# Performance work log

Measured on AMD Instinct MI355X. Metric: run time of the kernel, lower is better.

## Reference

```python
import jax, jax.numpy as jnp
import numpy as np
import math

N_NODES = 50000
N_EDGES = 800000
IN_DIM = 128
OUT_DIM = 64
TIME_DIM = 128


def setup_inputs() -> dict:
    key = jax.random.key(0)
    ks = jax.random.split(key, 9)
    return {
        "node_feats": jax.random.normal(ks[0], (N_NODES, IN_DIM), dtype=jnp.float32),
        "time_diff": jax.random.uniform(ks[1], (N_EDGES,), dtype=jnp.float32),
        "src": jax.random.randint(ks[2], (N_EDGES,), 0, N_NODES, dtype=jnp.int32),
        "dst": jax.random.randint(ks[3], (N_EDGES,), 0, N_NODES, dtype=jnp.int32),
        "W": jax.random.normal(ks[4], (OUT_DIM, IN_DIM), dtype=jnp.float32) * 0.05,
        "Wv": jax.random.normal(ks[5], (OUT_DIM, IN_DIM), dtype=jnp.float32) * 0.05,
        "omega": jax.random.normal(ks[6], (TIME_DIM // 2,), dtype=jnp.float32),
        "Wt": jax.random.normal(ks[7], (OUT_DIM, TIME_DIM), dtype=jnp.float32) * 0.05,
        "a": jax.random.normal(ks[8], (3 * OUT_DIM,), dtype=jnp.float32) * 0.05,
    }


def reference(node_feats, time_diff, src, dst, W, Wv, omega, Wt, a):
    N = node_feats.shape[0]
    d = W.shape[0]  # out_dim
    time_dim = 2 * omega.shape[0]

    # gather + linear projections per edge
    h_src = node_feats[src] @ W.T          # [E, d]
    h_dst = node_feats[dst] @ W.T          # [E, d]
    v_src = node_feats[src] @ Wv.T         # [E, d]

    # temporal encoding: interleaved sin/cos of t * omega, scaled by sqrt(1/dim)
    ang = time_diff[:, None] * omega[None, :]                       # [E, dim/2]
    pe = jnp.stack([jnp.sin(ang), jnp.cos(ang)], axis=-1)
    pe = pe.reshape(ang.shape[0], time_dim) * jnp.float32(math.sqrt(1.0 / time_dim))
    t_emb = pe @ Wt.T                                               # [E, d]

    # attn_fc(concat([h_src, h_dst, t_emb])) == split dot products (same math, no big concat)
    e = h_src @ a[:d] + h_dst @ a[d:2 * d] + t_emb @ a[2 * d:]      # [E]
    e = jnp.where(e > 0, e, 0.2 * e)  # LeakyReLU(0.2)

    # edge_softmax: softmax over incoming edges of each destination node
    m = jax.ops.segment_max(e, dst, num_segments=N)
    ex = jnp.exp(e - m[dst])
    den = jax.ops.segment_sum(ex, dst, num_segments=N)
    alpha = ex / den[dst]  # dropout is identity in eval mode

    # weighted message scatter-sum aggregation
    msg = v_src * alpha[:, None]                                    # [E, d]
    return jax.ops.segment_sum(msg, dst, num_segments=N)            # [N, d]
```

## Files before the change

kernel.cpp:

```cpp
#include <hip/hip_runtime.h>
#include <hip/hip_bf16.h>
#include <hip/hip_fp16.h>
#include <math.h>

#define IN_DIM   128
#define OUT_DIM  64
#define THALF    64
#define PE_SCALE 0.08838834764831845f
#define TBL      2048

typedef __attribute__((ext_vector_type(8))) short  short8;
typedef __attribute__((ext_vector_type(4))) float  f32x4;

__device__ inline unsigned short bf16_rne(float x) {
    unsigned u = __float_as_uint(x);
    return (unsigned short)((u + 0x7FFFu + ((u >> 16) & 1u)) >> 16);
}

__global__ __launch_bounds__(256) void k_prep(
    const float* __restrict__ W, const float* __restrict__ Wt,
    const float* __restrict__ a, const float* __restrict__ Wv,
    const float* __restrict__ omega,
    float* __restrict__ gtab, unsigned short* __restrict__ Bp,
    int* __restrict__ cnt, int* __restrict__ pref, int N)
{
    __shared__ float satv[IN_DIM];
    __shared__ float saW1[IN_DIM], saW2[IN_DIM];
    int t = threadIdx.x;
    if (t < IN_DIM) {
        float x3 = 0.f;
        for (int j = 0; j < OUT_DIM; ++j)
            x3 += a[2 * OUT_DIM + j] * Wt[j * IN_DIM + t];
        satv[t] = x3;
        if (blockIdx.x == 0) {
            float x1 = 0.f, x2 = 0.f;
            for (int j = 0; j < OUT_DIM; ++j) {
                float wj = W[j * IN_DIM + t];
                x1 += a[j] * wj;
                x2 += a[OUT_DIM + j] * wj;
            }
            saW1[t] = x1; saW2[t] = x2;
        }
    }
    __syncthreads();

    int idx = blockIdx.x * 256 + t;
    if (idx <= TBL) {
        float tt = (float)idx * (1.0f / TBL);
        float acc = 0.f;
#pragma unroll
        for (int i = 0; i < THALF; ++i) {
            float sp, cp;
            __sincosf(tt * omega[i], &sp, &cp);
            acc += sp * satv[2 * i] + cp * satv[2 * i + 1];
        }
        gtab[idx] = acc;
    }
    if (idx < 64) pref[idx] = 0;
    for (int i = idx; i < N; i += gridDim.x * 256) cnt[i] = 0;

    if (blockIdx.x == 0) {
        for (int i = t; i < 5 * 4 * 64 * 8; i += 256) {
            int j    = i & 7;
            int lane = (i >> 3) & 63;
            int k0i  = (i >> 9) & 3;
            int tt   = i >> 11;
            int kk = k0i * 32 + (lane >> 4) * 8 + j;
            int n  = lane & 15;
            float val;
            if (tt < 4)     val = Wv[(tt * 16 + n) * IN_DIM + kk];
            else            val = (n == 0) ? saW1[kk] : (n == 1) ? saW2[kk] : 0.f;
            Bp[i] = bf16_rne(val);
        }
    }
}

__global__ __launch_bounds__(256) void k_node_mfma(
    const float* __restrict__ feats,
    const unsigned short* __restrict__ Bp,
    unsigned short* __restrict__ vb,
    float* __restrict__ s1,
    float* __restrict__ s2,
    int N)
{
    int gwave = (blockIdx.x * 256 + threadIdx.x) >> 6;
    int lane  = threadIdx.x & 63;
    int ntiles = (N + 15) >> 4;
    if (gwave >= ntiles) return;
    int row = lane & 15, quad = lane >> 4;
    int nodeA = gwave * 16 + row;
    int nodeL = nodeA < N ? nodeA : N - 1;

    const float* arow = feats + (size_t)nodeL * IN_DIM + quad * 8;
    short8 afrag[4];
#pragma unroll
    for (int k0i = 0; k0i < 4; ++k0i) {
        float4 fa = *(const float4*)(arow + k0i * 32);
        float4 fb = *(const float4*)(arow + k0i * 32 + 4);
        union { unsigned u[4]; short8 s; } cv;
        cv.u[0] = (__float_as_uint(fa.x) >> 16) | (__float_as_uint(fa.y) & 0xFFFF0000u);
        cv.u[1] = (__float_as_uint(fa.z) >> 16) | (__float_as_uint(fa.w) & 0xFFFF0000u);
        cv.u[2] = (__float_as_uint(fb.x) >> 16) | (__float_as_uint(fb.y) & 0xFFFF0000u);
        cv.u[3] = (__float_as_uint(fb.z) >> 16) | (__float_as_uint(fb.w) & 0xFFFF0000u);
        afrag[k0i] = cv.s;
    }

    const short8* B8 = (const short8*)Bp;
    f32x4 acc[5];
#pragma unroll
    for (int t = 0; t < 5; ++t) acc[t] = (f32x4){0.f, 0.f, 0.f, 0.f};
#pragma unroll
    for (int t = 0; t < 5; ++t) {
#pragma unroll
        for (int k0i = 0; k0i < 4; ++k0i)
            acc[t] = __builtin_amdgcn_mfma_f32_16x16x32_bf16(
                afrag[k0i], B8[(t * 4 + k0i) * 64 + lane], acc[t], 0, 0, 0);
    }

    int col = lane & 15;
    int baseNode = gwave * 16 + quad * 4;
#pragma unroll
    for (int r = 0; r < 4; ++r) {
        int nd = baseNode + r;
        if (nd < N) {
            unsigned short* vr = vb + (size_t)nd * OUT_DIM + col;
#pragma unroll
            for (int t = 0; t < 4; ++t) vr[t * 16] = bf16_rne(acc[t][r]);
            if (col == 0)      s1[nd] = acc[4][r];
            else if (col == 1) s2[nd] = acc[4][r];
        }
    }
}

__global__ __launch_bounds__(256) void k_logits_rank(
    const float* __restrict__ tdiff,
    const int* __restrict__ src,
    const int* __restrict__ dst,
    const float* __restrict__ gtab,
    const float* __restrict__ s1,
    const float* __restrict__ s2,
    int* __restrict__ cnt,
    int2* __restrict__ rp,
    int E)
{
    int base = (blockIdx.x * 256 + threadIdx.x) * 8;
    if (base >= E) return;
    if (base + 8 <= E) {
        int4   sa = *(const int4*)(src + base);
        int4   sb = *(const int4*)(src + base + 4);
        int4   da = *(const int4*)(dst + base);
        int4   db = *(const int4*)(dst + base + 4);
        float4 ta = *(const float4*)(tdiff + base);
        float4 tb = *(const float4*)(tdiff + base + 4);
        int s[8]   = {sa.x, sa.y, sa.z, sa.w, sb.x, sb.y, sb.z, sb.w};
        int d[8]   = {da.x, da.y, da.z, da.w, db.x, db.y, db.z, db.w};
        float tv[8] = {ta.x, ta.y, ta.z, ta.w, tb.x, tb.y, tb.z, tb.w};

        int rk[8];
#pragma unroll
        for (int i = 0; i < 8; ++i) rk[i] = atomicAdd(cnt + d[i], 1);

        unsigned pw[8];
#pragma unroll
        for (int i = 0; i < 8; ++i) {
            float a1 = s1[s[i]];
            float a2 = s2[d[i]];
            float x = tv[i] * (float)TBL;
            int i0 = (int)x;
            i0 = i0 < 0 ? 0 : (i0 > TBL - 1 ? TBL - 1 : i0);
            float fr = x - (float)i0;
            float ev = a1 + a2 + PE_SCALE * (gtab[i0] + fr * (gtab[i0 + 1] - gtab[i0]));
            ev = ev > 0.f ? ev : 0.2f * ev;
            pw[i] = ((unsigned)s[i] << 16) | (unsigned)__half_as_ushort(__float2half(ev));
        }
#pragma unroll
        for (int i = 0; i < 4; ++i)
            *(int4*)(rp + base + 2 * i) =
                make_int4(rk[2 * i], (int)pw[2 * i], rk[2 * i + 1], (int)pw[2 * i + 1]);
    } else {
        for (int e = base; e < E; ++e) {
            int s = src[e], d = dst[e];
            int rk = atomicAdd(cnt + d, 1);
            float a1 = s1[s], a2 = s2[d];
            float x = tdiff[e] * (float)TBL;
            int i0 = (int)x;
            i0 = i0 < 0 ? 0 : (i0 > TBL - 1 ? TBL - 1 : i0);
            float fr = x - (float)i0;
            float ev = a1 + a2 + PE_SCALE * (gtab[i0] + fr * (gtab[i0 + 1] - gtab[i0]));
            ev = ev > 0.f ? ev : 0.2f * ev;
            unsigned pw = ((unsigned)s << 16) | (unsigned)__half_as_ushort(__float2half(ev));
            rp[e] = make_int2(rk, (int)pw);
        }
    }
}

__global__ __launch_bounds__(256) void k_scan1(const int* __restrict__ cnt,
                                               int* __restrict__ offs,
                                               int* __restrict__ pref, int N)
{
    __shared__ int lds[256];
    int b = blockIdx.x, t = threadIdx.x;
    int base = b * 1024 + t * 4;
    int v0 = (base + 0 < N) ? cnt[base + 0] : 0;
    int v1 = (base + 1 < N) ? cnt[base + 1] : 0;
    int v2 = (base + 2 < N) ? cnt[base + 2] : 0;
    int v3 = (base + 3 < N) ? cnt[base + 3] : 0;
    int s = v0 + v1 + v2 + v3;
    lds[t] = s;
    __syncthreads();
    for (int off = 1; off < 256; off <<= 1) {
        int tmp = (t >= off) ? lds[t - off] : 0;
        __syncthreads();
        lds[t] += tmp;
        __syncthreads();
    }
    int ex = lds[t] - s;
    if (base + 0 < N) offs[base + 0] = ex;
    ex += v0;
    if (base + 1 < N) offs[base + 1] = ex;
    ex += v1;
    if (base + 2 < N) offs[base + 2] = ex;
    ex += v2;
    if (base + 3 < N) offs[base + 3] = ex;
    int total = lds[255];
    if (t > b && t < (int)gridDim.x) atomicAdd(pref + t, total);
}

__global__ __launch_bounds__(256) void k_scatter(
    const int* __restrict__ dst,
    const int2* __restrict__ rp,
    const int* __restrict__ offs,
    const int* __restrict__ pref,
    unsigned* __restrict__ payload,
    int E)
{
    int base = (blockIdx.x * 256 + threadIdx.x) * 8;
    if (base >= E) return;
    if (base + 8 <= E) {
        int4 da = *(const int4*)(dst + base);
        int4 db = *(const int4*)(dst + base + 4);
        int d[8] = {da.x, da.y, da.z, da.w, db.x, db.y, db.z, db.w};
        int4 v0 = *(const int4*)(rp + base);
        int4 v1 = *(const int4*)(rp + base + 2);
        int4 v2 = *(const int4*)(rp + base + 4);
        int4 v3 = *(const int4*)(rp + base + 6);
        int rk[8] = {v0.x, v0.z, v1.x, v1.z, v2.x, v2.z, v3.x, v3.z};
        int pw[8] = {v0.y, v0.w, v1.y, v1.w, v2.y, v2.w, v3.y, v3.w};
        int o[8];
#pragma unroll
        for (int i = 0; i < 8; ++i) o[i] = offs[d[i]] + pref[d[i] >> 10] + rk[i];
#pragma unroll
        for (int i = 0; i < 8; ++i) payload[o[i]] = (unsigned)pw[i];
    } else {
        for (int e = base; e < E; ++e) {
            int d = dst[e];
            int2 v = rp[e];
            payload[offs[d] + pref[d >> 10] + v.x] = (unsigned)v.y;
        }
    }
}

__global__ __launch_bounds__(256) void k_aggregate(
    const int* __restrict__ offs,
    const int* __restrict__ pref,
    const unsigned* __restrict__ payload,
    const unsigned short* __restrict__ vb,
    float* __restrict__ out,
    int N, int E)
{
    int wid  = (blockIdx.x * blockDim.x + threadIdx.x) >> 6;
    int lane = threadIdx.x & 63;
    if (wid >= N) return;
    int beg = offs[wid] + pref[wid >> 10];
    int end = (wid + 1 < N) ? (offs[wid + 1] + pref[(wid + 1) >> 10]) : E;
    int deg = end - beg;
    int g8 = lane >> 3, r = lane & 7;

    float acc[8];
#pragma unroll
    for (int i = 0; i < 8; ++i) acc[i] = 0.f;
    float den = 0.f;

    for (int base = 0; base < deg; base += 64) {
        int cl = deg - base; if (cl > 64) cl = 64;
        bool valid = lane < cl;
        unsigned pl = valid ? payload[beg + base + lane] : 0u;
        float ex = valid ? __expf(__half2float(__ushort_as_half((unsigned short)(pl & 0xFFFFu)))) : 0.f;
        int   sv = valid ? (int)(pl >> 16) : 0;

        float sum = ex;
#pragma unroll
        for (int off = 32; off; off >>= 1) sum += __shfl_xor(sum, off, 64);
        den += sum;

        int rounds = (cl + 15) >> 4;
        for (int j = 0; j < rounds; ++j) {
            int i0 = j * 16 + g8;
            int i1 = i0 + 8;
            float e0 = __shfl(ex, i0, 64);
            int   s0 = __shfl(sv, i0, 64);
            float e1 = __shfl(ex, i1, 64);
            int   s1v = __shfl(sv, i1, 64);
            uint4 w0 = *((const uint4*)(vb + (size_t)s0 * OUT_DIM) + r);
            uint4 w1 = *((const uint4*)(vb + (size_t)s1v * OUT_DIM) + r);
            acc[0] += e0 * __uint_as_float(w0.x << 16)         + e1 * __uint_as_float(w1.x << 16);
            acc[1] += e0 * __uint_as_float(w0.x & 0xFFFF0000u) + e1 * __uint_as_float(w1.x & 0xFFFF0000u);
            acc[2] += e0 * __uint_as_float(w0.y << 16)         + e1 * __uint_as_float(w1.y << 16);
            acc[3] += e0 * __uint_as_float(w0.y & 0xFFFF0000u) + e1 * __uint_as_float(w1.y & 0xFFFF0000u);
            acc[4] += e0 * __uint_as_float(w0.z << 16)         + e1 * __uint_as_float(w1.z << 16);
            acc[5] += e0 * __uint_as_float(w0.z & 0xFFFF0000u) + e1 * __uint_as_float(w1.z & 0xFFFF0000u);
            acc[6] += e0 * __uint_as_float(w0.w << 16)         + e1 * __uint_as_float(w1.w << 16);
            acc[7] += e0 * __uint_as_float(w0.w & 0xFFFF0000u) + e1 * __uint_as_float(w1.w & 0xFFFF0000u);
        }
    }

#pragma unroll
    for (int i = 0; i < 8; ++i) {
        acc[i] += __shfl_xor(acc[i], 8, 64);
        acc[i] += __shfl_xor(acc[i], 16, 64);
        acc[i] += __shfl_xor(acc[i], 32, 64);
    }

    if (g8 == 0) {
        float inv = (deg > 0) ? 1.f / den : 0.f;
        float* o = out + (size_t)wid * OUT_DIM + r * 8;
        *(float4*)(o)     = make_float4(acc[0] * inv, acc[1] * inv, acc[2] * inv, acc[3] * inv);
        *(float4*)(o + 4) = make_float4(acc[4] * inv, acc[5] * inv, acc[6] * inv, acc[7] * inv);
    }
}

extern "C" void kernel_launch(void* const* d_in, const int* in_sizes, int n_in,
                              void* d_out, int out_size, void* d_ws, size_t ws_size,
                              hipStream_t stream) {
    const float* feats = (const float*)d_in[0];
    const float* tdiff = (const float*)d_in[1];
    const int*   src   = (const int*)d_in[2];
    const int*   dst   = (const int*)d_in[3];
    const float* W     = (const float*)d_in[4];
    const float* Wv    = (const float*)d_in[5];
    const float* omega = (const float*)d_in[6];
    const float* Wt    = (const float*)d_in[7];
    const float* a     = (const float*)d_in[8];
    float* out = (float*)d_out;

    int N = in_sizes[0] / IN_DIM;
    int E = in_sizes[1];

    int offs_elems = ((N + 1 + 3) / 4) * 4;
    float* ws      = (float*)d_ws;
    unsigned short* vb = (unsigned short*)ws;
    float* s1      = ws + (size_t)N * 32;
    float* s2      = s1 + N;
    int2*  rp      = (int2*)(s2 + N);
    unsigned* payload = (unsigned*)(rp + E);
    int*   cnt     = (int*)(payload + E);
    int*   offs    = cnt + N;
    int*   pref    = offs + offs_elems;
    float* gtab    = (float*)(pref + 64);
    unsigned short* Bp = (unsigned short*)(gtab + TBL + 1);

    int nb = (N + 1023) / 1024;
    int ntiles = (N + 15) / 16;
    int eb8 = (E + 8 * 256 - 1) / (8 * 256);

    k_prep<<<64, 256, 0, stream>>>(W, Wt, a, Wv, omega, gtab, Bp, cnt, pref, N);
    k_node_mfma<<<(ntiles * 64 + 255) / 256, 256, 0, stream>>>(feats, Bp, vb, s1, s2, N);
    k_logits_rank<<<eb8, 256, 0, stream>>>(tdiff, src, dst, gtab, s1, s2, cnt, rp, E);
    k_scan1<<<nb, 256, 0, stream>>>(cnt, offs, pref, N);
    k_scatter<<<eb8, 256, 0, stream>>>(dst, rp, offs, pref, payload, E);
    long long tot = (long long)N * OUT_DIM;
    k_aggregate<<<(int)((tot + 255) / 256), 256, 0, stream>>>(offs, pref, payload, vb, out, N, E);
}
```

Baseline: 192.3 us.

## Replace global atomic ranking with per-block LDS histograms and fuse logits into scatter

Per-destination counts and ranks are now built from per-block shared-memory histograms (16-bit packed counters, 16K edges per block) instead of global atomics on a count array. A column scan then turns the per-block histograms into block base offsets. Logit computation is fused into the scatter kernel, which removes the intermediate rank/payload buffer. The cost is a B×N histogram array in global memory (about 49×50000 words) that must be written, scanned and gathered randomly. Each block also needs 100KB of LDS, which limits occupancy to one block per CU.

```diff
diff --git a/kernel.cpp b/kernel.cpp
--- a/kernel.cpp
+++ b/kernel.cpp
@@ -8,6 +8,8 @@
 #define THALF    64
 #define PE_SCALE 0.08838834764831845f
 #define TBL      2048
+#define EPB_LOG  14
+#define EPB      (1 << EPB_LOG)
 
 typedef __attribute__((ext_vector_type(8))) short  short8;
 typedef __attribute__((ext_vector_type(4))) float  f32x4;
@@ -22,7 +24,7 @@
     const float* __restrict__ a, const float* __restrict__ Wv,
     const float* __restrict__ omega,
     float* __restrict__ gtab, unsigned short* __restrict__ Bp,
-    int* __restrict__ cnt, int* __restrict__ pref, int N)
+    int* __restrict__ pref)
 {
     __shared__ float satv[IN_DIM];
     __shared__ float saW1[IN_DIM], saW2[IN_DIM];
@@ -57,7 +59,6 @@
         gtab[idx] = acc;
     }
     if (idx < 64) pref[idx] = 0;
-    for (int i = idx; i < N; i += gridDim.x * 256) cnt[i] = 0;
 
     if (blockIdx.x == 0) {
         for (int i = t; i < 5 * 4 * 64 * 8; i += 256) {
@@ -75,122 +76,57 @@
     }
 }
 
-__global__ __launch_bounds__(256) void k_node_mfma(
-    const float* __restrict__ feats,
-    const unsigned short* __restrict__ Bp,
-    unsigned short* __restrict__ vb,
-    float* __restrict__ s1,
-    float* __restrict__ s2,
-    int N)
-{
-    int gwave = (blockIdx.x * 256 + threadIdx.x) >> 6;
-    int lane  = threadIdx.x & 63;
-    int ntiles = (N + 15) >> 4;
-    if (gwave >= ntiles) return;
-    int row = lane & 15, quad = lane >> 4;
-    int nodeA = gwave * 16 + row;
-    int nodeL = nodeA < N ? nodeA : N - 1;
-
-    const float* arow = feats + (size_t)nodeL * IN_DIM + quad * 8;
-    short8 afrag[4];
-#pragma unroll
-    for (int k0i = 0; k0i < 4; ++k0i) {
-        float4 fa = *(const float4*)(arow + k0i * 32);
-        float4 fb = *(const float4*)(arow + k0i * 32 + 4);
-        union { unsigned u[4]; short8 s; } cv;
-        cv.u[0] = (__float_as_uint(fa.x) >> 16) | (__float_as_uint(fa.y) & 0xFFFF0000u);
-        cv.u[1] = (__float_as_uint(fa.z) >> 16) | (__float_as_uint(fa.w) & 0xFFFF0000u);
-        cv.u[2] = (__float_as_uint(fb.x) >> 16) | (__float_as_uint(fb.y) & 0xFFFF0000u);
-        cv.u[3] = (__float_as_uint(fb.z) >> 16) | (__float_as_uint(fb.w) & 0xFFFF0000u);
-        afrag[k0i] = cv.s;
-    }
-
-    const short8* B8 = (const short8*)Bp;
-    f32x4 acc[5];
-#pragma unroll
-    for (int t = 0; t < 5; ++t) acc[t] = (f32x4){0.f, 0.f, 0.f, 0.f};
-#pragma unroll
-    for (int t = 0; t < 5; ++t) {
-#pragma unroll
-        for (int k0i = 0; k0i < 4; ++k0i)
-            acc[t] = __builtin_amdgcn_mfma_f32_16x16x32_bf16(
-                afrag[k0i], B8[(t * 4 + k0i) * 64 + lane], acc[t], 0, 0, 0);
-    }
-
-    int col = lane & 15;
-    int baseNode = gwave * 16 + quad * 4;
-#pragma unroll
-    for (int r = 0; r < 4; ++r) {
-        int nd = baseNode + r;
-        if (nd < N) {
-            unsigned short* vr = vb + (size_t)nd * OUT_DIM + col;
-#pragma unroll
-            for (int t = 0; t < 4; ++t) vr[t * 16] = bf16_rne(acc[t][r]);
-            if (col == 0)      s1[nd] = acc[4][r];
-            else if (col == 1) s2[nd] = acc[4][r];
-        }
-    }
-}
-
-__global__ __launch_bounds__(256) void k_logits_rank(
-    const float* __restrict__ tdiff,
-    const int* __restrict__ src,
+__global__ __launch_bounds__(1024) void k_hist(
     const int* __restrict__ dst,
-    const float* __restrict__ gtab,
-    const float* __restrict__ s1,
-    const float* __restrict__ s2,
-    int* __restrict__ cnt,
-    int2* __restrict__ rp,
-    int E)
-{
-    int base = (blockIdx.x * 256 + threadIdx.x) * 8;
-    if (base >= E) return;
-    if (base + 8 <= E) {
-        int4   sa = *(const int4*)(src + base);
-        int4   sb = *(const int4*)(src + base + 4);
-        int4   da = *(const int4*)(dst + base);
-        int4   db = *(const int4*)(dst + base + 4);
-        float4 ta = *(const float4*)(tdiff + base);
-        float4 tb = *(const float4*)(tdiff + base + 4);
-        int s[8]   = {sa.x, sa.y, sa.z, sa.w, sb.x, sb.y, sb.z, sb.w};
-        int d[8]   = {da.x, da.y, da.z, da.w, db.x, db.y, db.z, db.w};
-        float tv[8] = {ta.x, ta.y, ta.z, ta.w, tb.x, tb.y, tb.z, tb.w};
-
-        int rk[8];
-#pragma unroll
-        for (int i = 0; i < 8; ++i) rk[i] = atomicAdd(cnt + d[i], 1);
-
-        unsigned pw[8];
-#pragma unroll
-        for (int i = 0; i < 8; ++i) {
-            float a1 = s1[s[i]];
-            float a2 = s2[d[i]];
-            float x = tv[i] * (float)TBL;
-            int i0 = (int)x;
-            i0 = i0 < 0 ? 0 : (i0 > TBL - 1 ? TBL - 1 : i0);
-            float fr = x - (float)i0;
-            float ev = a1 + a2 + PE_SCALE * (gtab[i0] + fr * (gtab[i0 + 1] - gtab[i0]));
-            ev = ev > 0.f ? ev : 0.2f * ev;
-            pw[i] = ((unsigned)s[i] << 16) | (unsigned)__half_as_ushort(__float2half(ev));
-        }
-#pragma unroll
-        for (int i = 0; i < 4; ++i)
-            *(int4*)(rp + base + 2 * i) =
-                make_int4(rk[2 * i], (int)pw[2 * i], rk[2 * i + 1], (int)pw[2 * i + 1]);
+    unsigned short* __restrict__ lrank,
+    unsigned* __restrict__ ghist,
+    int N, int E)
+{
+    extern __shared__ unsigned h[];
+    int NH = (N + 1) >> 1;
+    int t = threadIdx.x;
+    for (int i = t; i < NH; i += 1024) h[i] = 0u;
+    __syncthreads();
+    int b = blockIdx.x;
+    int e0 = b << EPB_LOG;
+    int e1 = e0 + EPB; if (e1 > E) e1 = E;
+    for (int e = e0 + t; e < e1; e += 1024) {
+        int d = dst[e];
+        unsigned inc = (d & 1) ? 0x10000u : 1u;
+        unsigned old = atomicAdd(&h[d >> 1], inc);
+        lrank[e] = (unsigned short)((d & 1) ? (old >> 16) : (old & 0xFFFFu));
+    }
+    __syncthreads();
+    unsigned* gh = ghist + (size_t)b * N;
+    for (int w = t; w < NH; w += 1024) {
+        unsigned v = h[w];
+        int n0 = 2 * w;
+        if (n0 + 1 < N) *(uint2*)(gh + n0) = make_uint2(v & 0xFFFFu, v >> 16);
+        else            gh[n0] = v & 0xFFFFu;
+    }
+}
+
+__global__ __launch_bounds__(256) void k_scan_base(
+    unsigned* __restrict__ ghist, int* __restrict__ cnt, int B, int N)
+{
+    int n0 = (blockIdx.x * 256 + threadIdx.x) * 2;
+    if (n0 >= N) return;
+    if (n0 + 1 < N) {
+        unsigned r0 = 0, r1 = 0;
+        for (int b = 0; b < B; ++b) {
+            unsigned* p = ghist + (size_t)b * N + n0;
+            uint2 c = *(uint2*)p;
+            *(uint2*)p = make_uint2(r0, r1);
+            r0 += c.x; r1 += c.y;
+        }
+        *(int2*)(cnt + n0) = make_int2((int)r0, (int)r1);
     } else {
-        for (int e = base; e < E; ++e) {
-            int s = src[e], d = dst[e];
-            int rk = atomicAdd(cnt + d, 1);
-            float a1 = s1[s], a2 = s2[d];
-            float x = tdiff[e] * (float)TBL;
-            int i0 = (int)x;
-            i0 = i0 < 0 ? 0 : (i0 > TBL - 1 ? TBL - 1 : i0);
-            float fr = x - (float)i0;
-            float ev = a1 + a2 + PE_SCALE * (gtab[i0] + fr * (gtab[i0 + 1] - gtab[i0]));
-            ev = ev > 0.f ? ev : 0.2f * ev;
-            unsigned pw = ((unsigned)s << 16) | (unsigned)__half_as_ushort(__float2half(ev));
-            rp[e] = make_int2(rk, (int)pw);
-        }
+        unsigned r0 = 0;
+        for (int b = 0; b < B; ++b) {
+            unsigned* p = ghist + (size_t)b * N + n0;
+            unsigned c = *p; *p = r0; r0 += c;
+        }
+        cnt[n0] = (int)r0;
     }
 }
 
@@ -226,36 +162,117 @@
     if (t > b && t < (int)gridDim.x) atomicAdd(pref + t, total);
 }
 
-__global__ __launch_bounds__(256) void k_scatter(
+__global__ __launch_bounds__(256) void k_node_mfma(
+    const float* __restrict__ feats,
+    const unsigned short* __restrict__ Bp,
+    unsigned short* __restrict__ vb,
+    float* __restrict__ s1,
+    float* __restrict__ s2,
+    int N)
+{
+    int gwave = (blockIdx.x * 256 + threadIdx.x) >> 6;
+    int lane  = threadIdx.x & 63;
+    int ntiles = (N + 15) >> 4;
+    if (gwave >= ntiles) return;
+    int row = lane & 15, quad = lane >> 4;
+    int nodeA = gwave * 16 + row;
+    int nodeL = nodeA < N ? nodeA : N - 1;
+
+    const float* arow = feats + (size_t)nodeL * IN_DIM + quad * 8;
+    short8 afrag[4];
+#pragma unroll
+    for (int k0i = 0; k0i < 4; ++k0i) {
+        float4 fa = *(const float4*)(arow + k0i * 32);
+        float4 fb = *(const float4*)(arow + k0i * 32 + 4);
+        union { unsigned u[4]; short8 s; } cv;
+        cv.u[0] = (__float_as_uint(fa.x) >> 16) | (__float_as_uint(fa.y) & 0xFFFF0000u);
+        cv.u[1] = (__float_as_uint(fa.z) >> 16) | (__float_as_uint(fa.w) & 0xFFFF0000u);
+        cv.u[2] = (__float_as_uint(fb.x) >> 16) | (__float_as_uint(fb.y) & 0xFFFF0000u);
+        cv.u[3] = (__float_as_uint(fb.z) >> 16) | (__float_as_uint(fb.w) & 0xFFFF0000u);
+        afrag[k0i] = cv.s;
+    }
+
+    const short8* B8 = (const short8*)Bp;
+    f32x4 acc[5];
+#pragma unroll
+    for (int t = 0; t < 5; ++t) acc[t] = (f32x4){0.f, 0.f, 0.f, 0.f};
+#pragma unroll
+    for (int t = 0; t < 5; ++t) {
+#pragma unroll
+        for (int k0i = 0; k0i < 4; ++k0i)
+            acc[t] = __builtin_amdgcn_mfma_f32_16x16x32_bf16(
+                afrag[k0i], B8[(t * 4 + k0i) * 64 + lane], acc[t], 0, 0, 0);
+    }
+
+    int col = lane & 15;
+    int baseNode = gwave * 16 + quad * 4;
+#pragma unroll
+    for (int r = 0; r < 4; ++r) {
+        int nd = baseNode + r;
+        if (nd < N) {
+            unsigned short* vr = vb + (size_t)nd * OUT_DIM + col;
+#pragma unroll
+            for (int t = 0; t < 4; ++t) vr[t * 16] = bf16_rne(acc[t][r]);
+            if (col == 0)      s1[nd] = acc[4][r];
+            else if (col == 1) s2[nd] = acc[4][r];
+        }
+    }
+}
+
+__global__ __launch_bounds__(256) void k_scatter_fused(
+    const float* __restrict__ tdiff,
+    const int* __restrict__ src,
     const int* __restrict__ dst,
-    const int2* __restrict__ rp,
+    const float* __restrict__ gtab,
+    const float* __restrict__ s1,
+    const float* __restrict__ s2,
+    const unsigned short* __restrict__ lrank,
+    const unsigned* __restrict__ ghist,
     const int* __restrict__ offs,
     const int* __restrict__ pref,
     unsigned* __restrict__ payload,
-    int E)
-{
-    int base = (blockIdx.x * 256 + threadIdx.x) * 8;
+    int N, int E)
+{
+    int base = (blockIdx.x * 256 + threadIdx.x) * 4;
     if (base >= E) return;
-    if (base + 8 <= E) {
-        int4 da = *(const int4*)(dst + base);
-        int4 db = *(const int4*)(dst + base + 4);
-        int d[8] = {da.x, da.y, da.z, da.w, db.x, db.y, db.z, db.w};
-        int4 v0 = *(const int4*)(rp + base);
-        int4 v1 = *(const int4*)(rp + base + 2);
-        int4 v2 = *(const int4*)(rp + base + 4);
-        int4 v3 = *(const int4*)(rp + base + 6);
-        int rk[8] = {v0.x, v0.z, v1.x, v1.z, v2.x, v2.z, v3.x, v3.z};
-        int pw[8] = {v0.y, v0.w, v1.y, v1.w, v2.y, v2.w, v3.y, v3.w};
-        int o[8];
-#pragma unroll
-        for (int i = 0; i < 8; ++i) o[i] = offs[d[i]] + pref[d[i] >> 10] + rk[i];
-#pragma unroll
-        for (int i = 0; i < 8; ++i) payload[o[i]] = (unsigned)pw[i];
+    if (base + 4 <= E) {
+        int4   s4 = *(const int4*)(src + base);
+        int4   d4 = *(const int4*)(dst + base);
+        float4 t4 = *(const float4*)(tdiff + base);
+        ushort4 l4 = *(const ushort4*)(lrank + base);
+        int s[4]    = {s4.x, s4.y, s4.z, s4.w};
+        int d[4]    = {d4.x, d4.y, d4.z, d4.w};
+        float tv[4] = {t4.x, t4.y, t4.z, t4.w};
+        int lr[4]   = {l4.x, l4.y, l4.z, l4.w};
+#pragma unroll
+        for (int i = 0; i < 4; ++i) {
+            float a1 = s1[s[i]];
+            float a2 = s2[d[i]];
+            float x = tv[i] * (float)TBL;
+            int i0 = (int)x;
+            i0 = i0 < 0 ? 0 : (i0 > TBL - 1 ? TBL - 1 : i0);
+            float fr = x - (float)i0;
+            float ev = a1 + a2 + PE_SCALE * (gtab[i0] + fr * (gtab[i0 + 1] - gtab[i0]));
+            ev = ev > 0.f ? ev : 0.2f * ev;
+            unsigned pw = ((unsigned)s[i] << 16) | (unsigned)__half_as_ushort(__float2half(ev));
+            int b = (base + i) >> EPB_LOG;
+            int pos = offs[d[i]] + pref[d[i] >> 10] + (int)ghist[(size_t)b * N + d[i]] + lr[i];
+            payload[pos] = pw;
+        }
     } else {
         for (int e = base; e < E; ++e) {
-            int d = dst[e];
-            int2 v = rp[e];
-            payload[offs[d] + pref[d >> 10] + v.x] = (unsigned)v.y;
+            int s = src[e], d = dst[e];
+            float a1 = s1[s], a2 = s2[d];
+            float x = tdiff[e] * (float)TBL;
+            int i0 = (int)x;
+            i0 = i0 < 0 ? 0 : (i0 > TBL - 1 ? TBL - 1 : i0);
+            float fr = x - (float)i0;
+            float ev = a1 + a2 + PE_SCALE * (gtab[i0] + fr * (gtab[i0 + 1] - gtab[i0]));
+            ev = ev > 0.f ? ev : 0.2f * ev;
+            unsigned pw = ((unsigned)s << 16) | (unsigned)__half_as_ushort(__float2half(ev));
+            int b = e >> EPB_LOG;
+            int pos = offs[d] + pref[d >> 10] + (int)ghist[(size_t)b * N + d] + (int)lrank[e];
+            payload[pos] = pw;
         }
     }
 }
@@ -345,29 +362,36 @@
 
     int N = in_sizes[0] / IN_DIM;
     int E = in_sizes[1];
+    int B = (E + EPB - 1) >> EPB_LOG;
 
     int offs_elems = ((N + 1 + 3) / 4) * 4;
     float* ws      = (float*)d_ws;
     unsigned short* vb = (unsigned short*)ws;
     float* s1      = ws + (size_t)N * 32;
     float* s2      = s1 + N;
-    int2*  rp      = (int2*)(s2 + N);
-    unsigned* payload = (unsigned*)(rp + E);
-    int*   cnt     = (int*)(payload + E);
+    unsigned* payload = (unsigned*)(s2 + N);
+    unsigned short* lrank = (unsigned short*)(payload + E);
+    int*   cnt     = (int*)(lrank + ((E + 1) & ~1));
     int*   offs    = cnt + N;
     int*   pref    = offs + offs_elems;
     float* gtab    = (float*)(pref + 64);
     unsigned short* Bp = (unsigned short*)(gtab + TBL + 1);
+    size_t gho = ((size_t)(Bp + 10240) - (size_t)ws) / 4;
+    gho = (gho + 1) & ~(size_t)1;
+    unsigned* ghist = (unsigned*)ws + gho;
 
     int nb = (N + 1023) / 1024;
     int ntiles = (N + 15) / 16;
-    int eb8 = (E + 8 * 256 - 1) / (8 * 256);
-
-    k_prep<<<64, 256, 0, stream>>>(W, Wt, a, Wv, omega, gtab, Bp, cnt, pref, N);
+    int eb4 = (E + 4 * 256 - 1) / (4 * 256);
+    unsigned ldsb = (unsigned)(((N + 1) / 2) * 4);
+
+    k_prep<<<(TBL / 256) + 1, 256, 0, stream>>>(W, Wt, a, Wv, omega, gtab, Bp, pref);
+    k_hist<<<B, 1024, ldsb, stream>>>(dst, lrank, ghist, N, E);
     k_node_mfma<<<(ntiles * 64 + 255) / 256, 256, 0, stream>>>(feats, Bp, vb, s1, s2, N);
-    k_logits_rank<<<eb8, 256, 0, stream>>>(tdiff, src, dst, gtab, s1, s2, cnt, rp, E);
+    k_scan_base<<<((N + 1) / 2 + 255) / 256, 256, 0, stream>>>(ghist, cnt, B, N);
     k_scan1<<<nb, 256, 0, stream>>>(cnt, offs, pref, N);
-    k_scatter<<<eb8, 256, 0, stream>>>(dst, rp, offs, pref, payload, E);
+    k_scatter_fused<<<eb4, 256, 0, stream>>>(tdiff, src, dst, gtab, s1, s2,
+                                             lrank, ghist, offs, pref, payload, N, E);
     long long tot = (long long)N * OUT_DIM;
     k_aggregate<<<(int)((tot + 255) / 256), 256, 0, stream>>>(offs, pref, payload, vb, out, N, E);
 }
```

Result: no change. 191.7 us (-0.3%).
